# Optimization experiments

Hardware: AMD Instinct MI355X
Metric: run time of the kernel (lower is better)

The kernel has to match this reference:

```python
import jax, jax.numpy as jnp
import numpy as np

H = 512  # h_dim = d_rnn


def _pair_mlp(paragraph, W1, W2):
    """Fused equivalent of: cat(p_i, p_j) @ W1 -> ReLU -> @ W2 -> ReLU.
    Splits W1 so the [B,n,n,2h] concatenated input is never materialized
    before the first GEMM.  paragraph: [B, n, H]; W1: [2H, 2H]; W2: [2H, d_pair].
    Returns [B, n, n, d_pair].
    """
    u = paragraph @ W1[:H]   # [B, n, 2H]  (contribution of p_i, broadcast over j)
    v = paragraph @ W1[H:]   # [B, n, 2H]  (contribution of p_j, broadcast over i)
    z = jax.nn.relu(u[:, :, None, :] + v[:, None, :, :])  # [B, n, n, 2H]
    return jax.nn.relu(z @ W2)  # [B, n, n, d_pair]  (dropout = identity in eval)


def reference(paragraph, Wf1, Wf2, w3, Wh1a, Wh1b, wl1, Wh2a, Wh2b, wl2):
    # rela_encode -> future MLP, then directional probs via w3
    rela_vec = _pair_mlp(paragraph, Wf1, Wf2)            # [B,n,n,d_pair]
    rela_p = jax.nn.softmax(rela_vec @ w3, axis=-1)      # [B,n,n,2]
    rela_vec_diret = jnp.concatenate((rela_vec, rela_p), axis=-1)

    # encode_history -> hist_left1 / hist_left2 MLPs and their heads
    hist1 = _pair_mlp(paragraph, Wh1a, Wh1b)
    hist2 = _pair_mlp(paragraph, Wh2a, Wh2b)
    left1_p = jax.nn.softmax(hist1 @ wl1, axis=-1)
    left2_p = jax.nn.softmax(hist2 @ wl2, axis=-1)
    hist_vec_left1 = jnp.concatenate((hist1, left1_p), axis=-1)
    hist_vec_left2 = jnp.concatenate((hist2, left2_p), axis=-1)

    # pack all rela_pred outputs into one tensor: [B, n, n, 3*(d_pair+2)]
    return jnp.concatenate((rela_vec_diret, hist_vec_left1, hist_vec_left2), axis=-1)


def setup_inputs() -> dict:
    key = jax.random.key(0)
    ks = jax.random.split(key, 10)
    B, N, d_pair = 4, 128, 256
    s1 = 1.0 / np.sqrt(2 * H)
    s2 = 1.0 / np.sqrt(d_pair)
    return {
        "paragraph": jax.random.normal(ks[0], (B, N, H), jnp.float32),
        "Wf1": jax.random.normal(ks[1], (2 * H, 2 * H), jnp.float32) * s1,
        "Wf2": jax.random.normal(ks[2], (2 * H, d_pair), jnp.float32) * s1,
        "w3": jax.random.normal(ks[3], (d_pair, 2), jnp.float32) * s2,
        "Wh1a": jax.random.normal(ks[4], (2 * H, 2 * H), jnp.float32) * s1,
        "Wh1b": jax.random.normal(ks[5], (2 * H, d_pair), jnp.float32) * s1,
        "wl1": jax.random.normal(ks[6], (d_pair, 2), jnp.float32) * s2,
        "Wh2a": jax.random.normal(ks[7], (2 * H, 2 * H), jnp.float32) * s1,
        "Wh2b": jax.random.normal(ks[8], (2 * H, d_pair), jnp.float32) * s1,
        "wl2": jax.random.normal(ks[9], (d_pair, 2), jnp.float32) * s2,
    }
```

## Files before the change

kernel.cpp:

```cpp
#include <hip/hip_runtime.h>


typedef __attribute__((ext_vector_type(4))) float floatx4;
typedef __attribute__((ext_vector_type(2))) float floatx2;
typedef __attribute__((ext_vector_type(8))) short short8;

#define KT 16
#define LSTRIDE 68
#define MB (1u << 20)

__device__ __forceinline__ void gload_lds16(const void* g, void* l) {
  __builtin_amdgcn_global_load_lds(
      (const __attribute__((address_space(1))) void*)g,
      (__attribute__((address_space(3))) void*)l, 16, 0, 0);
}

__device__ __forceinline__ void split8(const float* x, short8& hi, short8& lo) {
  unsigned hb[8], lb[8];
#pragma unroll
  for (int e = 0; e < 8; e++) {
    unsigned xb = __float_as_uint(x[e]);
    unsigned h = xb & 0xFFFF0000u;
    float l = x[e] - __uint_as_float(h);
    hb[e] = h;
    lb[e] = __float_as_uint(l) & 0xFFFF0000u;
  }
  union U { unsigned u[4]; short8 s; };
  U H, L;
#pragma unroll
  for (int p = 0; p < 4; p++) {
    H.u[p] = __builtin_amdgcn_perm(hb[2 * p + 1], hb[2 * p], 0x07060302u);
    L.u[p] = __builtin_amdgcn_perm(lb[2 * p + 1], lb[2 * p], 0x07060302u);
  }
  hi = H.s;
  lo = L.s;
}

__device__ __forceinline__ void make_frag(
    const floatx4& ua, const floatx4& ub,
    const floatx4& va, const floatx4& vb,
    short8& hi, short8& lo) {
  float z[8];
#pragma unroll
  for (int e = 0; e < 4; e++) {
    z[e] = fmaxf(ua[e] + va[e], 0.0f);
    z[4 + e] = fmaxf(ub[e] + vb[e], 0.0f);
  }
  split8(z, hi, lo);
}

__device__ __forceinline__ void prep_w1_body(
    int t, const float* __restrict__ W1, unsigned short* __restrict__ W1F) {
  int lane = t & 63;
  int nf = (t >> 6) & 127;
  int kt = t >> 13;
  int g = lane >> 4, c = lane & 15;
  int n = nf * 16 + c;
  int kbase = kt * 32 + g * 8;
  const float* src = W1 + (long)((n >= 1024 ? 512 : 0) + kbase) * 1024 + (n & 1023);

  unsigned hb[8], lb[8];
#pragma unroll
  for (int e = 0; e < 8; e++) {
    float w = src[(long)e * 1024];
    unsigned wb = __float_as_uint(w);
    unsigned h = wb & 0xFFFF0000u;
    float l = w - __uint_as_float(h);
    hb[e] = h;
    lb[e] = __float_as_uint(l) & 0xFFFF0000u;
  }
  union U { unsigned u[4]; short8 s; };
  U H, L;
#pragma unroll
  for (int p = 0; p < 4; p++) {
    H.u[p] = __builtin_amdgcn_perm(hb[2 * p + 1], hb[2 * p], 0x07060302u);
    L.u[p] = __builtin_amdgcn_perm(lb[2 * p + 1], lb[2 * p], 0x07060302u);
  }
  long base = ((long)kt * 128 + nf) * 2 * 64 + lane;
  *(short8*)(W1F + (base + 0) * 8) = H.s;
  *(short8*)(W1F + (base + 64) * 8) = L.s;
}

__device__ __forceinline__ void prep_w2_body(
    int t, const float* __restrict__ W2, unsigned short* __restrict__ W2F) {
  int lane = t & 63;
  int nf = (t >> 6) & 15;
  int kt = t >> 10;
  int g = lane >> 4, c = lane & 15;
  int n = nf * 16 + c;
  int kbase = kt * 32 + g * 8;

  unsigned hb[8], lb[8];
#pragma unroll
  for (int e = 0; e < 8; e++) {
    float w = W2[(long)(kbase + e) * 256 + n];
    unsigned wb = __float_as_uint(w);
    unsigned h = wb & 0xFFFF0000u;
    float l = w - __uint_as_float(h);
    hb[e] = h;
    lb[e] = __float_as_uint(l) & 0xFFFF0000u;
  }
  union U { unsigned u[4]; short8 s; };
  U H, L;
#pragma unroll
  for (int p = 0; p < 4; p++) {
    H.u[p] = __builtin_amdgcn_perm(hb[2 * p + 1], hb[2 * p], 0x07060302u);
    L.u[p] = __builtin_amdgcn_perm(lb[2 * p + 1], lb[2 * p], 0x07060302u);
  }
  long base = (((long)kt * 16 + nf) * 2) * 64 + lane;
  *(short8*)(W2F + (base + 0) * 8) = H.s;
  *(short8*)(W2F + (base + 64) * 8) = L.s;
}

__global__ __launch_bounds__(256) void prep_all(
    const float* __restrict__ Wf1, const float* __restrict__ Wh1a,
    const float* __restrict__ Wh2a, const float* __restrict__ Wf2,
    const float* __restrict__ Wh1b, const float* __restrict__ Wh2b,
    unsigned short* __restrict__ w1f_all, unsigned short* __restrict__ w2f_all) {
  int bx = blockIdx.x;
  if (bx < 1536) {
    int mlp = bx >> 9;
    const float* W1 = (mlp == 0) ? Wf1 : (mlp == 1) ? Wh1a : Wh2a;
    prep_w1_body((bx & 511) * 256 + threadIdx.x, W1,
                 w1f_all + (long)mlp * (2 * MB));
  } else {
    int bb = bx - 1536;
    int mlp = bb >> 7;
    const float* W2 = (mlp == 0) ? Wf2 : (mlp == 1) ? Wh1b : Wh2b;
    prep_w2_body((bb & 127) * 256 + threadIdx.x, W2,
                 w2f_all + (long)mlp * (MB / 2));
  }
}

__device__ __forceinline__ void stage1_core(
    int bx, const float* __restrict__ P,
    const unsigned short* __restrict__ W1F,
    float* __restrict__ uF, float* __restrict__ vF) {
  int m0 = (bx >> 4) * 16;
  int n0 = (bx & 15) * 128;
  int tid = threadIdx.x;
  int wid = tid >> 6, lane = tid & 63;
  int g = lane >> 4, r = lane & 15;
  int nw0 = n0 + wid * 32;

  const float* prow = P + (long)(m0 + r) * 512;

  floatx4 acc[2];
#pragma unroll
  for (int nf = 0; nf < 2; nf++) acc[nf] = (floatx4){0.f, 0.f, 0.f, 0.f};

  for (int kt = 0; kt < 16; kt++) {
    int k0 = kt * 32 + g * 8;
    float a[8];
    floatx4 a0 = *(const floatx4*)(prow + k0);
    floatx4 a1 = *(const floatx4*)(prow + k0 + 4);
#pragma unroll
    for (int e = 0; e < 4; e++) { a[e] = a0[e]; a[4 + e] = a1[e]; }
    short8 ahi, alo;
    split8(a, ahi, alo);
#pragma unroll
    for (int nf = 0; nf < 2; nf++) {
      int nfg = (nw0 >> 4) + nf;
      const unsigned short* wp = W1F + (((long)kt * 128 + nfg) * 2 * 64 + lane) * 8;
      short8 whi = *(const short8*)wp;
      short8 wlo = *(const short8*)(wp + 64 * 8);
      acc[nf] = __builtin_amdgcn_mfma_f32_16x16x32_bf16(ahi, whi, acc[nf], 0, 0, 0);
      acc[nf] = __builtin_amdgcn_mfma_f32_16x16x32_bf16(alo, whi, acc[nf], 0, 0, 0);
      acc[nf] = __builtin_amdgcn_mfma_f32_16x16x32_bf16(ahi, wlo, acc[nf], 0, 0, 0);
    }
  }
  if (n0 < 1024) {
#pragma unroll
    for (int nf = 0; nf < 2; nf++)
#pragma unroll
      for (int reg = 0; reg < 4; reg++)
        uF[(long)(m0 + g * 4 + reg) * 1024 + nw0 + nf * 16 + r] = acc[nf][reg];
  } else {
    int kt = (nw0 - 1024) >> 5;
    long base = ((long)((m0 >> 7) * 32 + kt) * 8 + ((m0 >> 4) & 7)) * 512;
#pragma unroll
    for (int nf = 0; nf < 2; nf++) {
      int gt = nf * 2 + (r >> 3);
#pragma unroll
      for (int reg = 0; reg < 4; reg++)
        vF[base + (gt * 16 + g * 4 + reg) * 8 + (r & 7)] = acc[nf][reg];
    }
  }
}

__global__ __launch_bounds__(256) void stage1_mfma3(
    const float* __restrict__ P, const unsigned short* __restrict__ w1f_all,
    float* __restrict__ uF_all, float* __restrict__ vF_all) {
  int mlp = blockIdx.x >> 9;
  stage1_core(blockIdx.x & 511, P, w1f_all + (long)mlp * (2 * MB),
              uF_all + (long)mlp * 524288, vF_all + (long)mlp * 524288);
}

__global__ __launch_bounds__(512, 4) void pair_mfma3(
    const float* __restrict__ uF_all, const float* __restrict__ vF_all,
    const unsigned short* __restrict__ w2f_all,
    const float* __restrict__ w3_0, const float* __restrict__ w3_1,
    const float* __restrict__ w3_2, float* __restrict__ out) {
  __shared__ unsigned short wbuf[2][16384];
  int orig = blockIdx.x;
  int id = (orig & 7) * 192 + (orig >> 3);
  int mlp = id >> 9;
  int bi = id & 511;
  int b = bi >> 7;
  const float* w3 = (mlp == 0) ? w3_0 : (mlp == 1) ? w3_1 : w3_2;
  const float* uF = uF_all + (long)mlp * 524288;
  const float* vF = vF_all + (long)mlp * 524288;
  const unsigned short* W2F = w2f_all + (long)mlp * 524288;

  int tid = threadIdx.x;
  int wid = tid >> 6;
  int lane = tid & 63;
  int jq = wid >> 1;
  int nh = wid & 1;
  int g = lane >> 4;
  int r = lane & 15;

  const float* urow = uF + (long)bi * 1024;
  long vb0 = ((long)b * 32 * 8 + (jq * 2 + 0)) * 512 + lane * 8;
  long vb1 = ((long)b * 32 * 8 + (jq * 2 + 1)) * 512 + lane * 8;

  floatx4 acc[2][8];
#pragma unroll
  for (int mm = 0; mm < 2; mm++)
#pragma unroll
    for (int nf = 0; nf < 8; nf++) acc[mm][nf] = (floatx4){0.f, 0.f, 0.f, 0.f};

#pragma unroll
  for (int i = 0; i < 4; i++)
    gload_lds16(W2F + (i * 512 + tid) * 8, &wbuf[0][(i * 512 + tid) * 8]);
  floatx4 u0c = *(const floatx4*)(urow + g * 8);
  floatx4 u1c = *(const floatx4*)(urow + g * 8 + 4);
  floatx4 va0c[2], va1c[2];
  va0c[0] = *(const floatx4*)(vF + vb0);
  va1c[0] = *(const floatx4*)(vF + vb0 + 4);
  va0c[1] = *(const floatx4*)(vF + vb1);
  va1c[1] = *(const floatx4*)(vF + vb1 + 4);
  __syncthreads();

  int cur = 0;
  for (int kt = 0; kt < 32; kt++) {
    if (kt < 31) {
      const unsigned short* gs = W2F + (long)(kt + 1) * 16384;
#pragma unroll
      for (int i = 0; i < 4; i++)
        gload_lds16(gs + (i * 512 + tid) * 8, &wbuf[cur ^ 1][(i * 512 + tid) * 8]);
    }

    short8 ahi[2], alo[2];
    make_frag(u0c, u1c, va0c[0], va1c[0], ahi[0], alo[0]);
    make_frag(u0c, u1c, va0c[1], va1c[1], ahi[1], alo[1]);

    if (kt < 31) {
      int k0 = (kt + 1) * 32 + g * 8;
      long vo = (long)(kt + 1) * 8 * 512;
      u0c = *(const floatx4*)(urow + k0);
      u1c = *(const floatx4*)(urow + k0 + 4);
      va0c[0] = *(const floatx4*)(vF + vb0 + vo);
      va1c[0] = *(const floatx4*)(vF + vb0 + vo + 4);
      va0c[1] = *(const floatx4*)(vF + vb1 + vo);
      va1c[1] = *(const floatx4*)(vF + vb1 + vo + 4);
    }

    __builtin_amdgcn_s_setprio(1);
#pragma unroll
    for (int nf = 0; nf < 8; nf++) {
      const unsigned short* wp = &wbuf[cur][((nh * 8 + nf) * 2) * 512 + lane * 8];
      short8 whi = *(const short8*)wp;
      short8 wlo = *(const short8*)(wp + 512);
#pragma unroll
      for (int mm = 0; mm < 2; mm++) {
        acc[mm][nf] = __builtin_amdgcn_mfma_f32_16x16x32_bf16(
            ahi[mm], whi, acc[mm][nf], 0, 0, 0);
        acc[mm][nf] = __builtin_amdgcn_mfma_f32_16x16x32_bf16(
            alo[mm], whi, acc[mm][nf], 0, 0, 0);
        acc[mm][nf] = __builtin_amdgcn_mfma_f32_16x16x32_bf16(
            ahi[mm], wlo, acc[mm][nf], 0, 0, 0);
      }
    }
    __builtin_amdgcn_s_setprio(0);
    __syncthreads();
    cur ^= 1;
  }

  float* ps = (float*)wbuf;
  float* ob = out + (long)(bi * 128) * 774 + mlp * 258;
  floatx2 w3v[8];
#pragma unroll
  for (int nf = 0; nf < 8; nf++)
    w3v[nf] = *(const floatx2*)(w3 + ((nh * 8 + nf) * 16 + r) * 2);
#pragma unroll
  for (int mm = 0; mm < 2; mm++) {
#pragma unroll
    for (int reg = 0; reg < 4; reg++) {
      int row = jq * 32 + mm * 16 + g * 4 + reg;
      float* orow = ob + (long)row * 774 + nh * 128;
      float s0 = 0.f, s1 = 0.f;
#pragma unroll
      for (int nf = 0; nf < 8; nf++) {
        float y = acc[mm][nf][reg];
        y = y > 0.f ? y : 0.f;
        orow[nf * 16 + r] = y;
        s0 += y * w3v[nf][0];
        s1 += y * w3v[nf][1];
      }
#pragma unroll
      for (int off = 1; off < 16; off <<= 1) {
        s0 += __shfl_xor(s0, off, 64);
        s1 += __shfl_xor(s1, off, 64);
      }
      if (r == 0) {
        ps[row * 4 + nh * 2 + 0] = s0;
        ps[row * 4 + nh * 2 + 1] = s1;
      }
    }
  }
  __syncthreads();
  if (tid < 128) {
    int row = tid;
    float s0 = ps[row * 4 + 0] + ps[row * 4 + 2];
    float s1 = ps[row * 4 + 1] + ps[row * 4 + 3];
    float m = fmaxf(s0, s1);
    float e0 = __expf(s0 - m), e1 = __expf(s1 - m);
    float inv = 1.0f / (e0 + e1);
    floatx2 pr;
    pr[0] = e0 * inv;
    pr[1] = e1 * inv;
    *(floatx2*)(ob + (long)row * 774 + 256) = pr;
  }
}

__global__ __launch_bounds__(256) void stage1_valu(
    const float* __restrict__ P, const float* __restrict__ W1,
    float* __restrict__ uv) {
  __shared__ float at[KT][LSTRIDE];
  __shared__ float wt[KT][LSTRIDE];
  int bx = blockIdx.x;
  int m0 = (bx >> 5) * 64;
  int c0 = (bx & 31) * 64;
  int half = c0 >> 10;
  int ccol = c0 & 1023;
  int tid = threadIdx.x;
  int tm = tid >> 4, tn = tid & 15;
  int lm = tid >> 2;
  int lk4 = (tid & 3) * 4;
  int lkk = tid >> 4;
  int lc4 = (tid & 15) * 4;

  float acc[4][4] = {};

  for (int k0 = 0; k0 < 512; k0 += KT) {
    floatx4 pa = *(const floatx4*)(P + (long)(m0 + lm) * 512 + k0 + lk4);
    floatx4 wa = *(const floatx4*)(W1 + (long)(half * 512 + k0 + lkk) * 1024 + ccol + lc4);
    __syncthreads();
#pragma unroll
    for (int e = 0; e < 4; e++) at[lk4 + e][lm] = pa[e];
    *(floatx4*)&wt[lkk][lc4] = wa;
    __syncthreads();
#pragma unroll
    for (int kk = 0; kk < KT; kk++) {
      floatx4 av = *(const floatx4*)&at[kk][tm * 4];
      floatx4 wv = *(const floatx4*)&wt[kk][tn * 4];
#pragma unroll
      for (int mm = 0; mm < 4; mm++)
#pragma unroll
        for (int nn = 0; nn < 4; nn++)
          acc[mm][nn] += av[mm] * wv[nn];
    }
  }
#pragma unroll
  for (int mm = 0; mm < 4; mm++) {
    floatx4 o;
#pragma unroll
    for (int nn = 0; nn < 4; nn++) o[nn] = acc[mm][nn];
    *(floatx4*)(uv + (long)(m0 + tm * 4 + mm) * 2048 + c0 + tn * 4) = o;
  }
}

__global__ __launch_bounds__(256) void pair_valu(
    const float* __restrict__ uv, const float* __restrict__ W2,
    float* __restrict__ out, int mlp) {
  __shared__ float zt[KT][LSTRIDE];
  __shared__ float wt[KT][LSTRIDE];
  int bx = blockIdx.x;
  int nb = bx & 3;
  int jh = (bx >> 2) & 1;
  int bi = bx >> 3;
  int b = bi >> 7;
  int j0 = jh * 64;
  int n0 = nb * 64;
  int tid = threadIdx.x;
  int tm = tid >> 4, tn = tid & 15;
  int lj = tid >> 2;
  int lk4 = (tid & 3) * 4;
  int lkk = tid >> 4;
  int ln4 = (tid & 15) * 4;

  const float* urow = uv + (long)bi * 2048;
  const float* vrow = uv + (long)(b * 128 + j0 + lj) * 2048 + 1024;

  float acc[4][4] = {};

  for (int k0 = 0; k0 < 1024; k0 += KT) {
    floatx4 uu = *(const floatx4*)(urow + k0 + lk4);
    floatx4 vv = *(const floatx4*)(vrow + k0 + lk4);
    floatx4 wa = *(const floatx4*)(W2 + (long)(k0 + lkk) * 256 + n0 + ln4);
    __syncthreads();
#pragma unroll
    for (int e = 0; e < 4; e++) {
      float z = uu[e] + vv[e];
      zt[lk4 + e][lj] = z > 0.f ? z : 0.f;
    }
    *(floatx4*)&wt[lkk][ln4] = wa;
    __syncthreads();
#pragma unroll
    for (int kk = 0; kk < KT; kk++) {
      floatx4 zv = *(const floatx4*)&zt[kk][tm * 4];
      floatx4 wv = *(const floatx4*)&wt[kk][tn * 4];
#pragma unroll
      for (int mm = 0; mm < 4; mm++)
#pragma unroll
        for (int nn = 0; nn < 4; nn++)
          acc[mm][nn] += zv[mm] * wv[nn];
    }
  }
  float* ob = out + (long)(bi * 128 + j0) * 774 + mlp * 258 + n0 + tn * 4;
#pragma unroll
  for (int mm = 0; mm < 4; mm++) {
    float* orow = ob + (long)(tm * 4 + mm) * 774;
    floatx2 pa, pb;
    pa[0] = acc[mm][0] > 0.f ? acc[mm][0] : 0.f;
    pa[1] = acc[mm][1] > 0.f ? acc[mm][1] : 0.f;
    pb[0] = acc[mm][2] > 0.f ? acc[mm][2] : 0.f;
    pb[1] = acc[mm][3] > 0.f ? acc[mm][3] : 0.f;
    *(floatx2*)orow = pa;
    *(floatx2*)(orow + 2) = pb;
  }
}

__global__ __launch_bounds__(256) void head_kernel(
    const float* __restrict__ w3_0, const float* __restrict__ w3_1,
    const float* __restrict__ w3_2, float* out) {
  int wid = threadIdx.x >> 6, lane = threadIdx.x & 63;
  int r = blockIdx.x * 4 + wid;
  int mlp = r >> 16;
  int row = r & 65535;
  const float* w3 = (mlp == 0) ? w3_0 : (mlp == 1) ? w3_1 : w3_2;
  const float* yp = out + (long)row * 774 + mlp * 258 + lane * 4;
  floatx2 ya = *(const floatx2*)yp;
  floatx2 yb = *(const floatx2*)(yp + 2);
  const float* wp = w3 + lane * 8;
  floatx4 wv0 = *(const floatx4*)wp;
  floatx4 wv1 = *(const floatx4*)(wp + 4);
  float s0 = ya[0] * wv0[0] + ya[1] * wv0[2] + yb[0] * wv1[0] + yb[1] * wv1[2];
  float s1 = ya[0] * wv0[1] + ya[1] * wv0[3] + yb[0] * wv1[1] + yb[1] * wv1[3];
#pragma unroll
  for (int off = 32; off > 0; off >>= 1) {
    s0 += __shfl_xor(s0, off, 64);
    s1 += __shfl_xor(s1, off, 64);
  }
  if (lane == 0) {
    float m = fmaxf(s0, s1);
    float e0 = __expf(s0 - m), e1 = __expf(s1 - m);
    float inv = 1.0f / (e0 + e1);
    floatx2 pr;
    pr[0] = e0 * inv;
    pr[1] = e1 * inv;
    *(floatx2*)(out + (long)row * 774 + mlp * 258 + 256) = pr;
  }
}

extern "C" void kernel_launch(void* const* d_in, const int* in_sizes, int n_in,
                              void* d_out, int out_size, void* d_ws, size_t ws_size,
                              hipStream_t stream) {
  const float* para = (const float*)d_in[0];
  const float* Wf1  = (const float*)d_in[1];
  const float* Wf2  = (const float*)d_in[2];
  const float* w3   = (const float*)d_in[3];
  const float* Wh1a = (const float*)d_in[4];
  const float* Wh1b = (const float*)d_in[5];
  const float* wl1  = (const float*)d_in[6];
  const float* Wh2a = (const float*)d_in[7];
  const float* Wh2b = (const float*)d_in[8];
  const float* wl2  = (const float*)d_in[9];

  float* outp = (float*)d_out;

  if (ws_size >= (size_t)27 * MB) {
    float* uF_all = (float*)d_ws;
    float* vF_all = (float*)((char*)d_ws + 6 * MB);
    unsigned short* w2f_all = (unsigned short*)((char*)d_ws + 12 * MB);
    unsigned short* w1f_all = (unsigned short*)((char*)d_ws + 15 * MB);
    prep_all<<<1920, 256, 0, stream>>>(Wf1, Wh1a, Wh2a, Wf2, Wh1b, Wh2b,
                                       w1f_all, w2f_all);
    stage1_mfma3<<<1536, 256, 0, stream>>>(para, w1f_all, uF_all, vF_all);
    pair_mfma3<<<1536, 512, 0, stream>>>(uF_all, vF_all, w2f_all,
                                         w3, wl1, wl2, outp);
  } else {
    const float* W1s[3] = {Wf1, Wh1a, Wh2a};
    const float* W2s[3] = {Wf2, Wh1b, Wh2b};
    float* uv = (float*)d_ws;
    for (int mlp = 0; mlp < 3; mlp++) {
      stage1_valu<<<256, 256, 0, stream>>>(para, W1s[mlp], uv);
      pair_valu<<<4096, 256, 0, stream>>>(uv, W2s[mlp], outp, mlp);
    }
    head_kernel<<<49152, 256, 0, stream>>>(w3, wl1, wl2, outp);
  }
}
```

Measured before the change: 473.6 us.

## Switch pair GEMM to 32x32x16 MFMA with reworked W2/v layouts

Moves the pair-stage GEMM from 16x16x32 to 32x32x16 bf16 MFMA tiles, with four 32-wide accumulator tiles per wave. The W2 prep and the v output layout of stage 1 are reordered to match the new fragment shapes. The u row is preloaded into LDS once instead of being streamed from global each k-step, and the k-loop is unrolled by two so the double buffers are addressed statically. Larger MFMA tiles give more reuse per LDS operand load and fewer instructions, but each wave now holds 64 accumulator floats. The epilogue reduction now spans 32 lanes.

```diff
diff --git a/kernel.cpp b/kernel.cpp
--- a/kernel.cpp
+++ b/kernel.cpp
@@ -3,6 +3,7 @@
 
 typedef __attribute__((ext_vector_type(4))) float floatx4;
 typedef __attribute__((ext_vector_type(2))) float floatx2;
+typedef __attribute__((ext_vector_type(16))) float floatx16;
 typedef __attribute__((ext_vector_type(8))) short short8;
 
 #define KT 16
@@ -81,14 +82,15 @@
   *(short8*)(W1F + (base + 64) * 8) = L.s;
 }
 
-__device__ __forceinline__ void prep_w2_body(
+__device__ __forceinline__ void prep_w2_body32(
     int t, const float* __restrict__ W2, unsigned short* __restrict__ W2F) {
   int lane = t & 63;
-  int nf = (t >> 6) & 15;
+  int ksub = (t >> 6) & 1;
+  int nf32 = (t >> 7) & 7;
   int kt = t >> 10;
-  int g = lane >> 4, c = lane & 15;
-  int n = nf * 16 + c;
-  int kbase = kt * 32 + g * 8;
+  int g2 = lane >> 5, c32 = lane & 31;
+  int n = nf32 * 32 + c32;
+  int kbase = kt * 32 + ksub * 16 + g2 * 8;
 
   unsigned hb[8], lb[8];
 #pragma unroll
@@ -107,9 +109,9 @@
     H.u[p] = __builtin_amdgcn_perm(hb[2 * p + 1], hb[2 * p], 0x07060302u);
     L.u[p] = __builtin_amdgcn_perm(lb[2 * p + 1], lb[2 * p], 0x07060302u);
   }
-  long base = (((long)kt * 16 + nf) * 2) * 64 + lane;
+  long base = ((((long)kt * 8 + nf32) * 2) * 2 + ksub) * 64 + lane;
   *(short8*)(W2F + (base + 0) * 8) = H.s;
-  *(short8*)(W2F + (base + 64) * 8) = L.s;
+  *(short8*)(W2F + (base + 128) * 8) = L.s;
 }
 
 __global__ __launch_bounds__(256) void prep_all(
@@ -127,8 +129,8 @@
     int bb = bx - 1536;
     int mlp = bb >> 7;
     const float* W2 = (mlp == 0) ? Wf2 : (mlp == 1) ? Wh1b : Wh2b;
-    prep_w2_body((bb & 127) * 256 + threadIdx.x, W2,
-                 w2f_all + (long)mlp * (MB / 2));
+    prep_w2_body32((bb & 127) * 256 + threadIdx.x, W2,
+                   w2f_all + (long)mlp * (MB / 2));
   }
 }
 
@@ -177,13 +179,17 @@
         uF[(long)(m0 + g * 4 + reg) * 1024 + nw0 + nf * 16 + r] = acc[nf][reg];
   } else {
     int kt = (nw0 - 1024) >> 5;
-    long base = ((long)((m0 >> 7) * 32 + kt) * 8 + ((m0 >> 4) & 7)) * 512;
 #pragma unroll
     for (int nf = 0; nf < 2; nf++) {
-      int gt = nf * 2 + (r >> 3);
-#pragma unroll
-      for (int reg = 0; reg < 4; reg++)
-        vF[base + (gt * 16 + g * 4 + reg) * 8 + (r & 7)] = acc[nf][reg];
+#pragma unroll
+      for (int reg = 0; reg < 4; reg++) {
+        int m = m0 + g * 4 + reg;
+        int b = m >> 7;
+        int jf = (m >> 5) & 3;
+        long idx = (((long)(b * 32 + kt)) * 4 + jf) * 1024 +
+                   ((r >> 3) * 32 + (m & 31)) * 16 + nf * 8 + (r & 7);
+        vF[idx] = acc[nf][reg];
+      }
     }
   }
 }
@@ -196,12 +202,50 @@
               uF_all + (long)mlp * 524288, vF_all + (long)mlp * 524288);
 }
 
+#define PAIR_BODY(KTC, RBUF, SBUF)                                            \
+  {                                                                           \
+    const unsigned short* gs = W2F + (long)((KTC) + 1) * 16384;               \
+    _Pragma("unroll")                                                         \
+    for (int i = 0; i < 4; i++)                                               \
+      gload_lds16(gs + (i * 512 + tid) * 8, &(SBUF)[(i * 512 + tid) * 8]);    \
+    floatx4 u0 = *(const floatx4*)&ulds[(KTC) * 32 + g2 * 8];                 \
+    floatx4 u1 = *(const floatx4*)&ulds[(KTC) * 32 + g2 * 8 + 4];             \
+    floatx4 u2 = *(const floatx4*)&ulds[(KTC) * 32 + 16 + g2 * 8];            \
+    floatx4 u3 = *(const floatx4*)&ulds[(KTC) * 32 + 16 + g2 * 8 + 4];        \
+    short8 ahi0, alo0, ahi1, alo1;                                            \
+    make_frag(u0, u1, vc0, vc1, ahi0, alo0);                                  \
+    make_frag(u2, u3, vc2, vc3, ahi1, alo1);                                  \
+    vp += 4096;                                                               \
+    vc0 = *(const floatx4*)(vp);                                              \
+    vc1 = *(const floatx4*)(vp + 4);                                          \
+    vc2 = *(const floatx4*)(vp + 8);                                          \
+    vc3 = *(const floatx4*)(vp + 12);                                         \
+    __builtin_amdgcn_s_setprio(1);                                            \
+    _Pragma("unroll")                                                         \
+    for (int nf = 0; nf < 4; nf++) {                                          \
+      const unsigned short* wp = (RBUF) + (nh * 4 + nf) * 2048 + lane * 8;    \
+      short8 whi0 = *(const short8*)wp;                                       \
+      short8 whi1 = *(const short8*)(wp + 512);                               \
+      short8 wlo0 = *(const short8*)(wp + 1024);                              \
+      short8 wlo1 = *(const short8*)(wp + 1536);                              \
+      acc[nf] = __builtin_amdgcn_mfma_f32_32x32x16_bf16(ahi0, whi0, acc[nf], 0, 0, 0); \
+      acc[nf] = __builtin_amdgcn_mfma_f32_32x32x16_bf16(ahi1, whi1, acc[nf], 0, 0, 0); \
+      acc[nf] = __builtin_amdgcn_mfma_f32_32x32x16_bf16(alo0, whi0, acc[nf], 0, 0, 0); \
+      acc[nf] = __builtin_amdgcn_mfma_f32_32x32x16_bf16(alo1, whi1, acc[nf], 0, 0, 0); \
+      acc[nf] = __builtin_amdgcn_mfma_f32_32x32x16_bf16(ahi0, wlo0, acc[nf], 0, 0, 0); \
+      acc[nf] = __builtin_amdgcn_mfma_f32_32x32x16_bf16(ahi1, wlo1, acc[nf], 0, 0, 0); \
+    }                                                                         \
+    __builtin_amdgcn_s_setprio(0);                                            \
+    __syncthreads();                                                          \
+  }
+
 __global__ __launch_bounds__(512, 4) void pair_mfma3(
     const float* __restrict__ uF_all, const float* __restrict__ vF_all,
     const unsigned short* __restrict__ w2f_all,
     const float* __restrict__ w3_0, const float* __restrict__ w3_1,
     const float* __restrict__ w3_2, float* __restrict__ out) {
   __shared__ unsigned short wbuf[2][16384];
+  __shared__ float ulds[1024];
   int orig = blockIdx.x;
   int id = (orig & 7) * 192 + (orig >> 3);
   int mlp = id >> 9;
@@ -217,106 +261,61 @@
   int lane = tid & 63;
   int jq = wid >> 1;
   int nh = wid & 1;
-  int g = lane >> 4;
-  int r = lane & 15;
+  int g2 = lane >> 5;
+  int c32 = lane & 31;
+  int wj = jq * 32;
 
   const float* urow = uF + (long)bi * 1024;
-  long vb0 = ((long)b * 32 * 8 + (jq * 2 + 0)) * 512 + lane * 8;
-  long vb1 = ((long)b * 32 * 8 + (jq * 2 + 1)) * 512 + lane * 8;
-
-  floatx4 acc[2][8];
-#pragma unroll
-  for (int mm = 0; mm < 2; mm++)
-#pragma unroll
-    for (int nf = 0; nf < 8; nf++) acc[mm][nf] = (floatx4){0.f, 0.f, 0.f, 0.f};
-
+  if (tid < 256) gload_lds16(urow + tid * 4, &ulds[tid * 4]);
 #pragma unroll
   for (int i = 0; i < 4; i++)
     gload_lds16(W2F + (i * 512 + tid) * 8, &wbuf[0][(i * 512 + tid) * 8]);
-  floatx4 u0c = *(const floatx4*)(urow + g * 8);
-  floatx4 u1c = *(const floatx4*)(urow + g * 8 + 4);
-  floatx4 va0c[2], va1c[2];
-  va0c[0] = *(const floatx4*)(vF + vb0);
-  va1c[0] = *(const floatx4*)(vF + vb0 + 4);
-  va0c[1] = *(const floatx4*)(vF + vb1);
-  va1c[1] = *(const floatx4*)(vF + vb1 + 4);
+  const float* vp = vF + ((long)b * 32 * 4 + jq) * 1024 + lane * 16;
+  floatx4 vc0 = *(const floatx4*)(vp);
+  floatx4 vc1 = *(const floatx4*)(vp + 4);
+  floatx4 vc2 = *(const floatx4*)(vp + 8);
+  floatx4 vc3 = *(const floatx4*)(vp + 12);
+
+  floatx16 acc[4];
+#pragma unroll
+  for (int nf = 0; nf < 4; nf++)
+#pragma unroll
+    for (int e = 0; e < 16; e++) acc[nf][e] = 0.f;
+
   __syncthreads();
 
-  int cur = 0;
-  for (int kt = 0; kt < 32; kt++) {
-    if (kt < 31) {
-      const unsigned short* gs = W2F + (long)(kt + 1) * 16384;
-#pragma unroll
-      for (int i = 0; i < 4; i++)
-        gload_lds16(gs + (i * 512 + tid) * 8, &wbuf[cur ^ 1][(i * 512 + tid) * 8]);
-    }
-
-    short8 ahi[2], alo[2];
-    make_frag(u0c, u1c, va0c[0], va1c[0], ahi[0], alo[0]);
-    make_frag(u0c, u1c, va0c[1], va1c[1], ahi[1], alo[1]);
-
-    if (kt < 31) {
-      int k0 = (kt + 1) * 32 + g * 8;
-      long vo = (long)(kt + 1) * 8 * 512;
-      u0c = *(const floatx4*)(urow + k0);
-      u1c = *(const floatx4*)(urow + k0 + 4);
-      va0c[0] = *(const floatx4*)(vF + vb0 + vo);
-      va1c[0] = *(const floatx4*)(vF + vb0 + vo + 4);
-      va0c[1] = *(const floatx4*)(vF + vb1 + vo);
-      va1c[1] = *(const floatx4*)(vF + vb1 + vo + 4);
-    }
-
-    __builtin_amdgcn_s_setprio(1);
-#pragma unroll
-    for (int nf = 0; nf < 8; nf++) {
-      const unsigned short* wp = &wbuf[cur][((nh * 8 + nf) * 2) * 512 + lane * 8];
-      short8 whi = *(const short8*)wp;
-      short8 wlo = *(const short8*)(wp + 512);
-#pragma unroll
-      for (int mm = 0; mm < 2; mm++) {
-        acc[mm][nf] = __builtin_amdgcn_mfma_f32_16x16x32_bf16(
-            ahi[mm], whi, acc[mm][nf], 0, 0, 0);
-        acc[mm][nf] = __builtin_amdgcn_mfma_f32_16x16x32_bf16(
-            alo[mm], whi, acc[mm][nf], 0, 0, 0);
-        acc[mm][nf] = __builtin_amdgcn_mfma_f32_16x16x32_bf16(
-            ahi[mm], wlo, acc[mm][nf], 0, 0, 0);
-      }
-    }
-    __builtin_amdgcn_s_setprio(0);
-    __syncthreads();
-    cur ^= 1;
-  }
-
-  float* ps = (float*)wbuf;
+  for (int kt = 0; kt < 32; kt += 2) {
+    PAIR_BODY(kt, wbuf[1] - 16384, wbuf[1]);
+    PAIR_BODY(kt + 1, wbuf[1], wbuf[1] - 16384);
+  }
+
+  float* ps = ulds;
   float* ob = out + (long)(bi * 128) * 774 + mlp * 258;
-  floatx2 w3v[8];
-#pragma unroll
-  for (int nf = 0; nf < 8; nf++)
-    w3v[nf] = *(const floatx2*)(w3 + ((nh * 8 + nf) * 16 + r) * 2);
-#pragma unroll
-  for (int mm = 0; mm < 2; mm++) {
-#pragma unroll
-    for (int reg = 0; reg < 4; reg++) {
-      int row = jq * 32 + mm * 16 + g * 4 + reg;
-      float* orow = ob + (long)row * 774 + nh * 128;
-      float s0 = 0.f, s1 = 0.f;
-#pragma unroll
-      for (int nf = 0; nf < 8; nf++) {
-        float y = acc[mm][nf][reg];
-        y = y > 0.f ? y : 0.f;
-        orow[nf * 16 + r] = y;
-        s0 += y * w3v[nf][0];
-        s1 += y * w3v[nf][1];
-      }
-#pragma unroll
-      for (int off = 1; off < 16; off <<= 1) {
-        s0 += __shfl_xor(s0, off, 64);
-        s1 += __shfl_xor(s1, off, 64);
-      }
-      if (r == 0) {
-        ps[row * 4 + nh * 2 + 0] = s0;
-        ps[row * 4 + nh * 2 + 1] = s1;
-      }
+  floatx2 w3v[4];
+#pragma unroll
+  for (int nf = 0; nf < 4; nf++)
+    w3v[nf] = *(const floatx2*)(w3 + (nh * 128 + nf * 32 + c32) * 2);
+#pragma unroll
+  for (int reg = 0; reg < 16; reg++) {
+    int row = wj + (reg & 3) + 8 * (reg >> 2) + 4 * g2;
+    float* orow = ob + (long)row * 774 + nh * 128 + c32;
+    float s0 = 0.f, s1 = 0.f;
+#pragma unroll
+    for (int nf = 0; nf < 4; nf++) {
+      float y = acc[nf][reg];
+      y = y > 0.f ? y : 0.f;
+      orow[nf * 32] = y;
+      s0 += y * w3v[nf][0];
+      s1 += y * w3v[nf][1];
+    }
+#pragma unroll
+    for (int off = 1; off < 32; off <<= 1) {
+      s0 += __shfl_xor(s0, off, 64);
+      s1 += __shfl_xor(s1, off, 64);
+    }
+    if (c32 == 0) {
+      ps[row * 4 + nh * 2 + 0] = s0;
+      ps[row * 4 + nh * 2 + 1] = s1;
     }
   }
   __syncthreads();
```

Result: slower. 515.3 us (+8.8%).
